# Performance work log

Measured on AMD Instinct MI355X. Metric: run time of the kernel, lower is better.

The kernel has to match this reference:

```python
import jax, jax.numpy as jnp
import numpy as np

B = 256      # batch
D = 31       # per-mode feature dim (before bias-1 column)
FUSED = (D + 1) ** 3  # 32768
H1, H2, NCLS = 1024, 256, 4


def setup_inputs() -> dict:
    key = jax.random.key(0)
    ks = jax.random.split(key, 9)
    s = lambda fan_in: 1.0 / np.sqrt(fan_in)
    return {
        "x0": jax.random.normal(ks[0], (B, D), dtype=jnp.float32),
        "x1": jax.random.normal(ks[1], (B, D), dtype=jnp.float32),
        "x2": jax.random.normal(ks[2], (B, D), dtype=jnp.float32),
        "W1": jax.random.uniform(ks[3], (FUSED, H1), jnp.float32, -s(FUSED), s(FUSED)),
        "b1": jax.random.uniform(ks[4], (H1,), jnp.float32, -s(FUSED), s(FUSED)),
        "W2": jax.random.uniform(ks[5], (H1, H2), jnp.float32, -s(H1), s(H1)),
        "b2": jax.random.uniform(ks[6], (H2,), jnp.float32, -s(H1), s(H1)),
        "W3": jax.random.uniform(ks[7], (H2, NCLS), jnp.float32, -s(H2), s(H2)),
        "b3": jax.random.uniform(ks[8], (NCLS,), jnp.float32, -s(H2), s(H2)),
    }


def reference(x0, x1, x2, W1, b1, W2, b2, W3, b3):
    ones = jnp.ones((x0.shape[0], 1), dtype=x0.dtype)
    z0 = jnp.concatenate([x0, ones], axis=1)  # [B, D+1]
    z1 = jnp.concatenate([x1, ones], axis=1)
    z2 = jnp.concatenate([x2, ones], axis=1)
    # Batched triple outer product (vectorized over B, replacing the per-sample loop)
    fused = jnp.einsum("bi,bj,bk->bijk", z0, z1, z2).reshape(x0.shape[0], -1)  # [B, (D+1)^3]
    h = jax.nn.relu(fused @ W1 + b1)
    h = jax.nn.relu(h @ W2 + b2)
    return h @ W3 + b3  # [B, NCLS]
```

## Files before the change

### kernel.cpp

```cpp
#include <hip/hip_runtime.h>


typedef _Float16 half8 __attribute__((ext_vector_type(8)));
typedef _Float16 half4 __attribute__((ext_vector_type(4)));
typedef _Float16 half2 __attribute__((ext_vector_type(2)));
typedef float f32x4 __attribute__((ext_vector_type(4)));
typedef float f32x2 __attribute__((ext_vector_type(2)));

#define KSPLIT 32

__global__ __launch_bounds__(1024, 4) void k1_gemm(
    const float* __restrict__ x0, const float* __restrict__ x1,
    const float* __restrict__ x2, const float* __restrict__ W1,
    _Float16* __restrict__ partial)
{
    __shared__ _Float16 z1L[256 * 36];
    __shared__ _Float16 tileF[2 * 128 * 32];

    const int tid  = threadIdx.x;
    const int nt   = blockIdx.x & 7;
    const int ks   = blockIdx.x >> 3;
    const int lane = tid & 63;
    const int w    = tid >> 6;
    const int nl   = lane & 15;
    const int g    = lane >> 4;
    const int mh   = w & 3;
    const int nw   = w >> 2;

    for (int idx = tid; idx < 256 * 32; idx += 1024) {
        int b = idx >> 5, j = idx & 31;
        z1L[b * 36 + j] = (_Float16)((j < 31) ? x1[b * 31 + j] : 1.0f);
    }

    half8 z2v[4];
#pragma unroll
    for (int ms = 0; ms < 4; ++ms) {
        int b = mh * 64 + ms * 16 + nl;
        float v0 = (ks < 31) ? x0[b * 31 + ks] : 1.0f;
#pragma unroll
        for (int e = 0; e < 8; ++e) {
            int kp = g * 8 + e;
            float v2 = (kp < 31) ? x2[b * 31 + kp] : 1.0f;
            z2v[ms][e] = (_Float16)(v0 * v2);
        }
    }

    const int c = lane;
    const float* gsrc = W1 + ((size_t)ks * 1024 + 2 * w) * 1024 + nt * 128 + 2 * c;
    const int kpw = w ^ ((c & 7) << 1);
    const int waddr0 = (2 * c) * 32 + kpw * 2;
    const int waddr1 = waddr0 + 32;

    int raddr[2][2];
#pragma unroll
    for (int ns = 0; ns < 2; ++ns) {
        int n = nw * 32 + ns * 16 + nl;
        int sw = ((n >> 1) & 7) << 1;
#pragma unroll
        for (int u = 0; u < 2; ++u)
            raddr[ns][u] = n * 32 + ((g * 4 + 2 * u) ^ sw) * 2;
    }

    f32x2 rA[2], rB[2];
    rA[0] = *(const f32x2*)gsrc;
    rB[0] = *(const f32x2*)(gsrc + 1024);
    rA[1] = *(const f32x2*)(gsrc + 32768);
    rB[1] = *(const f32x2*)(gsrc + 32768 + 1024);
    {
        half2 w0, w1;
        w0[0] = (_Float16)rA[0][0]; w0[1] = (_Float16)rB[0][0];
        w1[0] = (_Float16)rA[0][1]; w1[1] = (_Float16)rB[0][1];
        *(half2*)&tileF[waddr0] = w0;
        *(half2*)&tileF[waddr1] = w1;
    }
    __syncthreads();

    f32x4 acc[4][2] = {};
    half4 z1q[4];

#define STEP(T_, TT, LOADF, WRITEF)                                            \
    {                                                                          \
        if (LOADF) {                                                           \
            const float* gp = gsrc + (size_t)((T_) + 2) * 32768;               \
            rA[(TT) & 1] = *(const f32x2*)gp;                                  \
            rB[(TT) & 1] = *(const f32x2*)(gp + 1024);                         \
        }                                                                      \
        if ((TT) == 0) {                                                       \
            _Pragma("unroll")                                                  \
            for (int ms = 0; ms < 4; ++ms)                                     \
                z1q[ms] = *(const half4*)&z1L[(mh * 64 + ms * 16 + nl) * 36 + t0]; \
        }                                                                      \
        const _Float16* tb = &tileF[((TT) & 1) * 4096];                        \
        half4 lo0 = *(const half4*)&tb[raddr[0][0]];                           \
        half4 hi0 = *(const half4*)&tb[raddr[0][1]];                           \
        half4 lo1 = *(const half4*)&tb[raddr[1][0]];                           \
        half4 hi1 = *(const half4*)&tb[raddr[1][1]];                           \
        half8 bh0 = __builtin_shufflevector(lo0, hi0, 0,1,2,3,4,5,6,7);        \
        half8 bh1 = __builtin_shufflevector(lo1, hi1, 0,1,2,3,4,5,6,7);        \
        _Pragma("unroll")                                                      \
        for (int ms = 0; ms < 4; ++ms) {                                       \
            half8 a = z2v[ms] * z1q[ms][TT];                                   \
            acc[ms][0] = __builtin_amdgcn_mfma_f32_16x16x32_f16(a, bh0, acc[ms][0], 0, 0, 0); \
            acc[ms][1] = __builtin_amdgcn_mfma_f32_16x16x32_f16(a, bh1, acc[ms][1], 0, 0, 0); \
        }                                                                      \
        if (WRITEF) {                                                          \
            half2 w0, w1;                                                      \
            w0[0] = (_Float16)rA[((TT) + 1) & 1][0];                           \
            w0[1] = (_Float16)rB[((TT) + 1) & 1][0];                           \
            w1[0] = (_Float16)rA[((TT) + 1) & 1][1];                           \
            w1[1] = (_Float16)rB[((TT) + 1) & 1][1];                           \
            _Float16* tw = &tileF[(((TT) + 1) & 1) * 4096];                    \
            *(half2*)&tw[waddr0] = w0;                                         \
            *(half2*)&tw[waddr1] = w1;                                         \
        }                                                                      \
        asm volatile("s_waitcnt lgkmcnt(0)\n\ts_barrier" ::: "memory");        \
    }

    for (int grp = 0; grp < 7; ++grp) {
        const int t0 = grp * 4;
        STEP(t0 + 0, 0, 1, 1)
        STEP(t0 + 1, 1, 1, 1)
        STEP(t0 + 2, 2, 1, 1)
        STEP(t0 + 3, 3, 1, 1)
    }
    {
        const int t0 = 28;
        STEP(28, 0, 1, 1)
        STEP(29, 1, 1, 1)
        STEP(30, 2, 0, 1)
        STEP(31, 3, 0, 0)
    }
#undef STEP

    _Float16* pbase = partial + ((size_t)ks << 18);
#pragma unroll
    for (int ms = 0; ms < 4; ++ms)
#pragma unroll
        for (int ns = 0; ns < 2; ++ns) {
            int h = nt * 128 + nw * 32 + ns * 16 + nl;
            int b0 = mh * 64 + ms * 16 + g * 4;
#pragma unroll
            for (int r = 0; r < 4; ++r)
                pbase[(b0 + r) * 1024 + h] = (_Float16)acc[ms][ns][r];
        }
}

__global__ __launch_bounds__(256) void k2_reduce(
    const _Float16* __restrict__ partial, const float* __restrict__ b1,
    float* __restrict__ h1)
{
    int e2 = blockIdx.x * 256 + threadIdx.x;
    const half2* pv = (const half2*)partial;
    float s0 = 0.f, s1 = 0.f;
#pragma unroll
    for (int sp = 0; sp < KSPLIT; ++sp) {
        half2 v = pv[(size_t)sp * 131072 + e2];
        s0 += (float)v[0]; s1 += (float)v[1];
    }
    int h = (e2 * 2) & 1023;
    f32x2 o;
    o[0] = fmaxf(s0 + b1[h], 0.f);
    o[1] = fmaxf(s1 + b1[h + 1], 0.f);
    *(f32x2*)&h1[e2 * 2] = o;
}

__global__ __launch_bounds__(256) void k3_layer2(
    const float* __restrict__ h1, const float* __restrict__ W2,
    float* __restrict__ p2)
{
    __shared__ float h1t[32 * 129];
    __shared__ float w2t[128 * 65];
    const int tid = threadIdx.x;
    const int m0 = blockIdx.x * 32, n0 = blockIdx.y * 64, k0 = blockIdx.z * 128;

    for (int idx = tid; idx < 32 * 128; idx += 256) {
        int m = idx >> 7, kk = idx & 127;
        h1t[m * 129 + kk] = h1[(m0 + m) * 1024 + k0 + kk];
    }
    for (int idx = tid; idx < 128 * 64; idx += 256) {
        int kk = idx >> 6, n = idx & 63;
        w2t[kk * 65 + n] = W2[(k0 + kk) * 256 + n0 + n];
    }
    __syncthreads();

    const int tn = tid & 63, tm = tid >> 6;
    float acc[8] = {};
    for (int kk = 0; kk < 128; ++kk) {
        float wv = w2t[kk * 65 + tn];
#pragma unroll
        for (int r = 0; r < 8; ++r)
            acc[r] += h1t[(tm * 8 + r) * 129 + kk] * wv;
    }
#pragma unroll
    for (int r = 0; r < 8; ++r)
        p2[blockIdx.z * 65536 + (m0 + tm * 8 + r) * 256 + n0 + tn] = acc[r];
}

__global__ __launch_bounds__(256) void k4_final(
    const float* __restrict__ p2, const float* __restrict__ b2,
    const float* __restrict__ W3, const float* __restrict__ b3,
    float* __restrict__ out)
{
    __shared__ float pL[256 * 5];
    const int b = blockIdx.x, n = threadIdx.x;
    float s = 0.f;
#pragma unroll
    for (int sp = 0; sp < 8; ++sp) s += p2[sp * 65536 + b * 256 + n];
    float h2 = fmaxf(s + b2[n], 0.f);
#pragma unroll
    for (int ccls = 0; ccls < 4; ++ccls) pL[n * 5 + ccls] = h2 * W3[n * 4 + ccls];
    __syncthreads();

    const int lane = n & 63, w = n >> 6;
    float v = pL[lane * 5 + w] + pL[(lane + 64) * 5 + w] +
              pL[(lane + 128) * 5 + w] + pL[(lane + 192) * 5 + w];
#pragma unroll
    for (int off = 32; off > 0; off >>= 1) v += __shfl_down(v, off);
    if (lane == 0) out[b * 4 + w] = v + b3[w];
}

extern "C" void kernel_launch(void* const* d_in, const int* in_sizes, int n_in,
                              void* d_out, int out_size, void* d_ws, size_t ws_size,
                              hipStream_t stream)
{
    (void)in_sizes; (void)n_in; (void)out_size; (void)ws_size;
    const float* x0 = (const float*)d_in[0];
    const float* x1 = (const float*)d_in[1];
    const float* x2 = (const float*)d_in[2];
    const float* W1 = (const float*)d_in[3];
    const float* b1 = (const float*)d_in[4];
    const float* W2 = (const float*)d_in[5];
    const float* b2 = (const float*)d_in[6];
    const float* W3 = (const float*)d_in[7];
    const float* b3 = (const float*)d_in[8];
    float* out = (float*)d_out;

    _Float16* partial = (_Float16*)d_ws;
    float* h1 = (float*)((char*)d_ws + (size_t)KSPLIT * 262144 * 2);
    float* p2 = h1 + 262144;

    k1_gemm  <<<dim3(256),     dim3(1024), 0, stream>>>(x0, x1, x2, W1, partial);
    k2_reduce<<<dim3(512),     dim3(256),  0, stream>>>(partial, b1, h1);
    k3_layer2<<<dim3(8, 4, 8), dim3(256),  0, stream>>>(h1, W2, p2);
    k4_final <<<dim3(256),     dim3(256),  0, stream>>>(p2, b2, W3, b3, out);
}
```

Baseline: 53.63 us.

## Halve N-tile per block and deepen W1 prefetch to four-stage LDS ring

The layer-1 GEMM kernel now uses 512-thread blocks, each covering 64 output columns instead of 128, and launches 512 blocks instead of 256. W1 loads switch from paired float2 reads to four scalar float loads per thread per k-slab. Three slabs are kept in flight in registers and fed through a 4-buffer padded LDS ring, replacing the swizzled double buffer. The aim is more blocks for load balancing and deeper latency hiding on the W1 stream. The trade-offs are scalar global loads that may coalesce less well, more LDS use, and the x0/x2 and z1 setup now repeated across twice as many blocks.

After: 54.56 us. About the same (+1.7%).

```diff
diff --git a/kernel.cpp b/kernel.cpp
--- a/kernel.cpp
+++ b/kernel.cpp
@@ -9,25 +9,26 @@
 
 #define KSPLIT 32
 
-__global__ __launch_bounds__(1024, 4) void k1_gemm(
+__global__ __launch_bounds__(512, 4) void k1_gemm(
     const float* __restrict__ x0, const float* __restrict__ x1,
     const float* __restrict__ x2, const float* __restrict__ W1,
     _Float16* __restrict__ partial)
 {
     __shared__ _Float16 z1L[256 * 36];
-    __shared__ _Float16 tileF[2 * 128 * 32];
+    __shared__ _Float16 tile[4][64 * 36];
 
     const int tid  = threadIdx.x;
-    const int nt   = blockIdx.x & 7;
-    const int ks   = blockIdx.x >> 3;
+    const int nt   = blockIdx.x & 15;
+    const int ks   = blockIdx.x >> 4;
     const int lane = tid & 63;
     const int w    = tid >> 6;
     const int nl   = lane & 15;
     const int g    = lane >> 4;
-    const int mh   = w & 3;
-    const int nw   = w >> 2;
-
-    for (int idx = tid; idx < 256 * 32; idx += 1024) {
+    const int mh   = w >> 1;
+    const int nw   = w & 1;
+    const int n0   = nt * 64;
+
+    for (int idx = tid; idx < 256 * 32; idx += 512) {
         int b = idx >> 5, j = idx & 31;
         z1L[b * 36 + j] = (_Float16)((j < 31) ? x1[b * 31 + j] : 1.0f);
     }
@@ -45,56 +46,49 @@
         }
     }
 
-    const int c = lane;
-    const float* gsrc = W1 + ((size_t)ks * 1024 + 2 * w) * 1024 + nt * 128 + 2 * c;
-    const int kpw = w ^ ((c & 7) << 1);
-    const int waddr0 = (2 * c) * 32 + kpw * 2;
-    const int waddr1 = waddr0 + 32;
-
-    int raddr[2][2];
-#pragma unroll
-    for (int ns = 0; ns < 2; ++ns) {
-        int n = nw * 32 + ns * 16 + nl;
-        int sw = ((n >> 1) & 7) << 1;
-#pragma unroll
-        for (int u = 0; u < 2; ++u)
-            raddr[ns][u] = n * 32 + ((g * 4 + 2 * u) ^ sw) * 2;
-    }
-
-    f32x2 rA[2], rB[2];
-    rA[0] = *(const f32x2*)gsrc;
-    rB[0] = *(const f32x2*)(gsrc + 1024);
-    rA[1] = *(const f32x2*)(gsrc + 32768);
-    rB[1] = *(const f32x2*)(gsrc + 32768 + 1024);
+    const int sn = tid & 63;
+    const float* gp = W1 + ((size_t)ks * 1024 + 4 * w) * 1024 + n0 + sn;
+    const int woff = sn * 36 + 4 * w;
+
+    const int roff0 = (nw * 32 + nl) * 36 + g * 8;
+    const int roff1 = (nw * 32 + 16 + nl) * 36 + g * 8;
+
+    float rq[4][4];
+#pragma unroll
+    for (int s = 0; s < 3; ++s) {
+#pragma unroll
+        for (int q = 0; q < 4; ++q) rq[s][q] = gp[q * 1024];
+        gp += 32768;
+    }
     {
-        half2 w0, w1;
-        w0[0] = (_Float16)rA[0][0]; w0[1] = (_Float16)rB[0][0];
-        w1[0] = (_Float16)rA[0][1]; w1[1] = (_Float16)rB[0][1];
-        *(half2*)&tileF[waddr0] = w0;
-        *(half2*)&tileF[waddr1] = w1;
-    }
-    __syncthreads();
+        half2 h01, h23;
+        h01[0] = (_Float16)rq[0][0]; h01[1] = (_Float16)rq[0][1];
+        h23[0] = (_Float16)rq[0][2]; h23[1] = (_Float16)rq[0][3];
+        *(half2*)&tile[0][woff]     = h01;
+        *(half2*)&tile[0][woff + 2] = h23;
+    }
+    asm volatile("s_waitcnt lgkmcnt(0)\n\ts_barrier" ::: "memory");
 
     f32x4 acc[4][2] = {};
     half4 z1q[4];
 
-#define STEP(T_, TT, LOADF, WRITEF)                                            \
+#define STEP(TT, ISSUE, WRITE, T0)                                             \
     {                                                                          \
-        if (LOADF) {                                                           \
-            const float* gp = gsrc + (size_t)((T_) + 2) * 32768;               \
-            rA[(TT) & 1] = *(const f32x2*)gp;                                  \
-            rB[(TT) & 1] = *(const f32x2*)(gp + 1024);                         \
+        if (ISSUE) {                                                           \
+            _Pragma("unroll")                                                  \
+            for (int q = 0; q < 4; ++q) rq[((TT) + 3) & 3][q] = gp[q * 1024];  \
+            gp += 32768;                                                       \
         }                                                                      \
         if ((TT) == 0) {                                                       \
             _Pragma("unroll")                                                  \
             for (int ms = 0; ms < 4; ++ms)                                     \
-                z1q[ms] = *(const half4*)&z1L[(mh * 64 + ms * 16 + nl) * 36 + t0]; \
-        }                                                                      \
-        const _Float16* tb = &tileF[((TT) & 1) * 4096];                        \
-        half4 lo0 = *(const half4*)&tb[raddr[0][0]];                           \
-        half4 hi0 = *(const half4*)&tb[raddr[0][1]];                           \
-        half4 lo1 = *(const half4*)&tb[raddr[1][0]];                           \
-        half4 hi1 = *(const half4*)&tb[raddr[1][1]];                           \
+                z1q[ms] = *(const half4*)&z1L[(mh * 64 + ms * 16 + nl) * 36 + (T0)]; \
+        }                                                                      \
+        const _Float16* tb = &tile[(TT) & 3][0];                               \
+        half4 lo0 = *(const half4*)&tb[roff0];                                 \
+        half4 hi0 = *(const half4*)&tb[roff0 + 4];                             \
+        half4 lo1 = *(const half4*)&tb[roff1];                                 \
+        half4 hi1 = *(const half4*)&tb[roff1 + 4];                             \
         half8 bh0 = __builtin_shufflevector(lo0, hi0, 0,1,2,3,4,5,6,7);        \
         half8 bh1 = __builtin_shufflevector(lo1, hi1, 0,1,2,3,4,5,6,7);        \
         _Pragma("unroll")                                                      \
@@ -103,33 +97,29 @@
             acc[ms][0] = __builtin_amdgcn_mfma_f32_16x16x32_f16(a, bh0, acc[ms][0], 0, 0, 0); \
             acc[ms][1] = __builtin_amdgcn_mfma_f32_16x16x32_f16(a, bh1, acc[ms][1], 0, 0, 0); \
         }                                                                      \
-        if (WRITEF) {                                                          \
-            half2 w0, w1;                                                      \
-            w0[0] = (_Float16)rA[((TT) + 1) & 1][0];                           \
-            w0[1] = (_Float16)rB[((TT) + 1) & 1][0];                           \
-            w1[0] = (_Float16)rA[((TT) + 1) & 1][1];                           \
-            w1[1] = (_Float16)rB[((TT) + 1) & 1][1];                           \
-            _Float16* tw = &tileF[(((TT) + 1) & 1) * 4096];                    \
-            *(half2*)&tw[waddr0] = w0;                                         \
-            *(half2*)&tw[waddr1] = w1;                                         \
+        if (WRITE) {                                                           \
+            const float* s = rq[((TT) + 1) & 3];                               \
+            half2 h01, h23;                                                    \
+            h01[0] = (_Float16)s[0]; h01[1] = (_Float16)s[1];                  \
+            h23[0] = (_Float16)s[2]; h23[1] = (_Float16)s[3];                  \
+            _Float16* tw = &tile[((TT) + 1) & 3][0];                           \
+            *(half2*)&tw[woff]     = h01;                                      \
+            *(half2*)&tw[woff + 2] = h23;                                      \
         }                                                                      \
         asm volatile("s_waitcnt lgkmcnt(0)\n\ts_barrier" ::: "memory");        \
     }
 
     for (int grp = 0; grp < 7; ++grp) {
         const int t0 = grp * 4;
-        STEP(t0 + 0, 0, 1, 1)
-        STEP(t0 + 1, 1, 1, 1)
-        STEP(t0 + 2, 2, 1, 1)
-        STEP(t0 + 3, 3, 1, 1)
-    }
-    {
-        const int t0 = 28;
-        STEP(28, 0, 1, 1)
-        STEP(29, 1, 1, 1)
-        STEP(30, 2, 0, 1)
-        STEP(31, 3, 0, 0)
-    }
+        STEP(0, 1, 1, t0)
+        STEP(1, 1, 1, t0)
+        STEP(2, 1, 1, t0)
+        STEP(3, 1, 1, t0)
+    }
+    STEP(0, 1, 1, 28)
+    STEP(1, 0, 1, 28)
+    STEP(2, 0, 1, 28)
+    STEP(3, 0, 0, 28)
 #undef STEP
 
     _Float16* pbase = partial + ((size_t)ks << 18);
@@ -137,7 +127,7 @@
     for (int ms = 0; ms < 4; ++ms)
 #pragma unroll
         for (int ns = 0; ns < 2; ++ns) {
-            int h = nt * 128 + nw * 32 + ns * 16 + nl;
+            int h = n0 + nw * 32 + ns * 16 + nl;
             int b0 = mh * 64 + ms * 16 + g * 4;
 #pragma unroll
             for (int r = 0; r < 4; ++r)
@@ -239,8 +229,8 @@
     float* h1 = (float*)((char*)d_ws + (size_t)KSPLIT * 262144 * 2);
     float* p2 = h1 + 262144;
 
-    k1_gemm  <<<dim3(256),     dim3(1024), 0, stream>>>(x0, x1, x2, W1, partial);
-    k2_reduce<<<dim3(512),     dim3(256),  0, stream>>>(partial, b1, h1);
-    k3_layer2<<<dim3(8, 4, 8), dim3(256),  0, stream>>>(h1, W2, p2);
-    k4_final <<<dim3(256),     dim3(256),  0, stream>>>(p2, b2, W3, b3, out);
-}
+    k1_gemm  <<<dim3(512),     dim3(512), 0, stream>>>(x0, x1, x2, W1, partial);
+    k2_reduce<<<dim3(512),     dim3(256), 0, stream>>>(partial, b1, h1);
+    k3_layer2<<<dim3(8, 4, 8), dim3(256), 0, stream>>>(h1, W2, p2);
+    k4_final <<<dim3(256),     dim3(256), 0, stream>>>(p2, b2, W3, b3, out);
+}
```
